# Performance work log

Hardware: AMD Instinct MI355X
Metric: run time of the kernel (lower is better)

Reference implementation:

```python
import jax, jax.numpy as jnp
import numpy as np

N_NODES = 50000
N_EDGES = 600000
VOCAB = 50000
D_IN = 256   # embed.output_size
D = 128      # size


def gcn_conv(x, w, b, src, dst, num_nodes):
    # PyG GCNConv: x' = D^{-1/2} (A + I) D^{-1/2} (x @ W^T) + b
    loop = jnp.arange(num_nodes)
    s = jnp.concatenate([src, loop])
    d = jnp.concatenate([dst, loop])
    x = x @ w.T                                           # [N, D]
    deg = jax.ops.segment_sum(jnp.ones_like(s, x.dtype), d, num_segments=num_nodes)
    dinv = jnp.where(deg > 0, jax.lax.rsqrt(deg), 0.0)
    norm = dinv[s] * dinv[d]                              # [E+N]
    msgs = x[s] * norm[:, None]                           # gather + scale
    out = jax.ops.segment_sum(msgs, d, num_segments=num_nodes)  # scatter-add
    return out + b


def setup_inputs() -> dict:
    key = jax.random.key(0)
    ks = jax.random.split(key, 7)
    node_tokens = jax.random.randint(ks[0], (N_NODES,), 0, VOCAB)
    edge_index = jax.random.randint(ks[1], (2, N_EDGES), 0, N_NODES)
    embed_table = jax.random.normal(ks[2], (VOCAB, D_IN), dtype=jnp.float32) * 0.02
    W_node_w = jax.random.normal(ks[3], (D, D_IN), dtype=jnp.float32) * 0.02
    W_node_b = jnp.zeros((D,), dtype=jnp.float32)
    w1 = jax.random.normal(ks[4], (D, D), dtype=jnp.float32) * 0.02
    b1 = jnp.zeros((D,), dtype=jnp.float32)
    w2 = jax.random.normal(ks[5], (D, D), dtype=jnp.float32) * 0.02
    b2 = jnp.zeros((D,), dtype=jnp.float32)
    return {"node_tokens": node_tokens, "edge_index": edge_index,
            "embed_table": embed_table, "W_node_w": W_node_w, "W_node_b": W_node_b,
            "w1": w1, "b1": b1, "w2": w2, "b2": b2}


def reference(node_tokens, edge_index, embed_table, W_node_w, W_node_b, w1, b1, w2, b2):
    src, dst = edge_index[0], edge_index[1]
    e = embed_table[node_tokens]                 # [N, D_IN] embedding lookup
    x = e @ W_node_w.T + W_node_b                # [N, D]
    x = gcn_conv(x, w1, b1, src, dst, N_NODES)
    x = jax.nn.relu(x)
    x = gcn_conv(x, w2, b2, src, dst, N_NODES)
    return x
```

## Files before the change

kernel.cpp:

```cpp
#include <hip/hip_runtime.h>
#include <hip/hip_bf16.h>

#define N_NODES 50000
#define N_EDGES 600000
#define D_IN 256
#define D 128

#define SCAN_CHUNK 1024
#define N_CHUNKS ((N_NODES + SCAN_CHUNK - 1) / SCAN_CHUNK)
#define GEMM_BLOCKS ((N_NODES + 31) / 32)
#define EDGE_BLOCKS ((N_EDGES + 255) / 256)

typedef unsigned short ushort_t;
typedef __attribute__((ext_vector_type(8))) short bf16x8;
typedef __attribute__((ext_vector_type(16))) float f32x16;

__device__ __forceinline__ float bf2f(ushort_t u) {
  union { unsigned int i; float f; } v;
  v.i = ((unsigned int)u) << 16;
  return v.f;
}
__device__ __forceinline__ ushort_t f2bf(float f) {
  union { float f; unsigned int i; } v;
  v.f = f;
  unsigned int x = v.i;
  unsigned int r = (x + 0x7FFFu + ((x >> 16) & 1u)) >> 16;
  return (ushort_t)r;
}
__device__ __forceinline__ float bflo(unsigned int u) {
  union { unsigned int i; float f; } v;
  v.i = u << 16;
  return v.f;
}
__device__ __forceinline__ float bfhi(unsigned int u) {
  union { unsigned int i; float f; } v;
  v.i = u & 0xFFFF0000u;
  return v.f;
}


__global__ __launch_bounds__(256) void k_prep_deg(
    const float* __restrict__ wn, const float* __restrict__ w1,
    const float* __restrict__ bn, const float* __restrict__ w2,
    const float* __restrict__ b1, const float* __restrict__ b2,
    const int* __restrict__ dst,
    ushort_t* __restrict__ WcSw, float* __restrict__ bc,
    ushort_t* __restrict__ W2Sw, float* __restrict__ b1f,
    float* __restrict__ b2f, int* __restrict__ deg,
    int* __restrict__ epos) {
  int bid = blockIdx.x;
  if (bid < 128) {
    int j = bid;
    int k = threadIdx.x;
    float acc = 0.f;
#pragma unroll 8
    for (int m = 0; m < 128; m++)
      acc += w1[j * 128 + m] * wn[m * 256 + k];
    ushort_t h = f2bf(acc);
    ushort_t l = f2bf(acc - bf2f(h));
    int wv = j >> 5, fm = j & 31;
    int kh = k >> 7, t = (k >> 4) & 7, fq = (k >> 3) & 1, c = k & 7;
    int lane = fq * 32 + fm;
    int base = ((wv * 2 + kh) * 8 + t) * 2 * 512 + lane * 8 + c;
    WcSw[base] = h;
    WcSw[base + 512] = l;
    if (k == 0) {
      float s = 0.f;
      for (int m = 0; m < 128; m++) s += w1[j * 128 + m] * bn[m];
      bc[j] = s;
    }
  } else if (bid < 193) {
    int i = (bid - 128) * 256 + threadIdx.x;
    if (i >= 16640) return;
    if (i < 16384) {
      float v = w2[i];
      ushort_t h = f2bf(v);
      ushort_t l = f2bf(v - bf2f(h));
      int j = i >> 7, k = i & 127;
      int wv = j >> 5, fm = j & 31;
      int t = (k >> 4) & 7, fq = (k >> 3) & 1, c = k & 7;
      int lane = fq * 32 + fm;
      int base = (wv * 8 + t) * 2 * 512 + lane * 8 + c;
      W2Sw[base] = h;
      W2Sw[base + 512] = l;
    } else if (i < 16512) {
      b1f[i - 16384] = b1[i - 16384];
    } else {
      b2f[i - 16512] = b2[i - 16512];
    }
  } else {
    int e = (bid - 193) * 256 + threadIdx.x;
    if (e < N_EDGES) epos[e] = atomicAdd(&deg[dst[e]], 1);
  }
}


__global__ void k_partial(const int* __restrict__ deg, int* __restrict__ partial) {
  __shared__ int lds[256];
  int b = blockIdx.x, t = threadIdx.x;
  int base = b * SCAN_CHUNK + t * 4;
  int s = 0;
#pragma unroll
  for (int i = 0; i < 4; i++) {
    int idx = base + i;
    if (idx < N_NODES) s += deg[idx];
  }
  lds[t] = s;
  __syncthreads();
  for (int off = 128; off > 0; off >>= 1) {
    if (t < off) lds[t] += lds[t + off];
    __syncthreads();
  }
  if (t == 0) partial[b] = lds[0];
}

__global__ void k_scan_final(const int* __restrict__ deg, const int* __restrict__ partial,
                             int* __restrict__ row_start, float* __restrict__ dinv,
                             ushort_t* __restrict__ T1z, ushort_t* __restrict__ T2z) {
  __shared__ int lds[256];
  __shared__ int plds[64];
  int b = blockIdx.x, t = threadIdx.x;
  if (t < N_CHUNKS) plds[t] = partial[t];
  __syncthreads();
  if (t == 0) {
    int s = 0;
    for (int i = 0; i < b; i++) s += plds[i];
    plds[63] = s;
  }
  int base = b * SCAN_CHUNK + t * 4;
  int v[4];
  int s = 0;
#pragma unroll
  for (int i = 0; i < 4; i++) {
    int idx = base + i;
    v[i] = (idx < N_NODES) ? deg[idx] : 0;
    s += v[i];
  }
  lds[t] = s;
  __syncthreads();
  for (int off = 1; off < 256; off <<= 1) {
    int add = (t >= off) ? lds[t - off] : 0;
    __syncthreads();
    lds[t] += add;
    __syncthreads();
  }
  int excl = lds[t] - s + plds[63];
#pragma unroll
  for (int i = 0; i < 4; i++) {
    int idx = base + i;
    if (idx < N_NODES) {
      row_start[idx] = excl;
      dinv[idx] = rsqrtf((float)(v[i] + 1));
      excl += v[i];
    }
  }
  if (b == 0) {
    if (t == 0) row_start[N_NODES] = N_EDGES;
    unsigned int* z1 = (unsigned int*)&T1z[(size_t)N_NODES * D];
    unsigned int* z2 = (unsigned int*)&T2z[(size_t)N_NODES * D];
    if (t < 64) z1[t] = 0u;
    else if (t < 128) z2[t - 64] = 0u;
  }
}

__global__ __launch_bounds__(256) void k_gemm_fill(
    const float* __restrict__ Xv, const int* __restrict__ tokens,
    const ushort_t* __restrict__ Wsw,
    const float* __restrict__ bias, const float* __restrict__ dinvp,
    ushort_t* __restrict__ OutT,
    const int* __restrict__ src, const int* __restrict__ dst,
    const int* __restrict__ row_start, const int* __restrict__ epos,
    int* __restrict__ csr) {
  constexpr int XS = 136;
  __shared__ __align__(16) ushort_t xh_lds[32 * XS];
  __shared__ __align__(16) ushort_t xl_lds[32 * XS];

  int bid = blockIdx.x;
  if (bid >= GEMM_BLOCKS) {
    int e = (bid - GEMM_BLOCKS) * 256 + threadIdx.x;
    if (e < N_EDGES) {
      int d = dst[e];
      csr[row_start[d] + epos[e]] = src[e];
    }
    return;
  }

  int tid = threadIdx.x;
  int lane = tid & 63;
  int wv = tid >> 6;
  int node0 = bid * 32;
  int fm = lane & 31;
  int fq = lane >> 5;
  int r8 = tid >> 5;
  int c32 = tid & 31;

  const char* xb = (const char*)Xv;
  float4 v0[4], v1[4];
  int rows[4];
#pragma unroll
  for (int i = 0; i < 4; i++) {
    rows[i] = r8 * 4 + i;
    int tk = tokens[min(node0 + rows[i], N_NODES - 1)];
    unsigned off = (unsigned)tk * (D_IN * 4) + (unsigned)c32 * 16;
    v0[i] = *(const float4*)(xb + off);
    v1[i] = *(const float4*)(xb + off + 512);
  }

  f32x16 acc;
#pragma unroll
  for (int r = 0; r < 16; r++) acc[r] = 0.f;

#pragma unroll
  for (int kh = 0; kh < 2; kh++) {
#pragma unroll
    for (int i = 0; i < 4; i++) {
      float4 v = (kh == 0) ? v0[i] : v1[i];
      ushort4 h, l;
      h.x = f2bf(v.x); l.x = f2bf(v.x - bf2f(h.x));
      h.y = f2bf(v.y); l.y = f2bf(v.y - bf2f(h.y));
      h.z = f2bf(v.z); l.z = f2bf(v.z - bf2f(h.z));
      h.w = f2bf(v.w); l.w = f2bf(v.w - bf2f(h.w));
      *(ushort4*)&xh_lds[rows[i] * XS + 4 * c32] = h;
      *(ushort4*)&xl_lds[rows[i] * XS + 4 * c32] = l;
    }
    __syncthreads();

    const ushort_t* wb = Wsw + ((size_t)(wv * 2 + kh) * 8) * 2 * 512 + lane * 8;
#pragma unroll
    for (int tc = 0; tc < 2; tc++) {
      bf16x8 wbh[4], wbl[4];
#pragma unroll
      for (int t4 = 0; t4 < 4; t4++) {
        wbh[t4] = *(const bf16x8*)(wb + (size_t)(tc * 4 + t4) * 1024);
        wbl[t4] = *(const bf16x8*)(wb + (size_t)(tc * 4 + t4) * 1024 + 512);
      }
#pragma unroll
      for (int t4 = 0; t4 < 4; t4++) {
        int ko = (tc * 4 + t4) * 16 + fq * 8;
        bf16x8 ah = *(const bf16x8*)&xh_lds[fm * XS + ko];
        bf16x8 al = *(const bf16x8*)&xl_lds[fm * XS + ko];
        acc = __builtin_amdgcn_mfma_f32_32x32x16_bf16(ah, wbh[t4], acc, 0, 0, 0);
        acc = __builtin_amdgcn_mfma_f32_32x32x16_bf16(ah, wbl[t4], acc, 0, 0, 0);
        acc = __builtin_amdgcn_mfma_f32_32x32x16_bf16(al, wbh[t4], acc, 0, 0, 0);
      }
    }
    if (kh == 0) __syncthreads();
  }

  int j = wv * 32 + fm;
  float bv = bias[j];
#pragma unroll
  for (int r = 0; r < 16; r++) {
    int row = (r & 3) + 8 * (r >> 2) + 4 * fq;
    int node = node0 + row;
    if (node < N_NODES)
      OutT[(size_t)node * D + j] = f2bf((acc[r] + bv) * dinvp[node]);
  }
}

__device__ __forceinline__ void addu4(float acc[8], uint4 u) {
  acc[0] += bflo(u.x);
  acc[1] += bfhi(u.x);
  acc[2] += bflo(u.y);
  acc[3] += bfhi(u.y);
  acc[4] += bflo(u.z);
  acc[5] += bfhi(u.z);
  acc[6] += bflo(u.w);
  acc[7] += bfhi(u.w);
}

__device__ __forceinline__ uint4 ldrow(const char* tbase, int s, int h) {
  return *(const uint4*)(tbase + (((unsigned)s << 8) + ((unsigned)h << 4)));
}

__device__ __forceinline__ void burst8(const char* tbase, int sidx,
                                       int gbase, int qoff, int h, float acc[8]) {
  uint4 u[8];
#pragma unroll
  for (int q = 0; q < 8; q++) {
    int s = __shfl(sidx, gbase + qoff + q);
    u[q] = ldrow(tbase, s, h);
  }
#pragma unroll
  for (int q = 0; q < 8; q++) addu4(acc, u[q]);
}

__device__ __forceinline__ void agg_tail(const char* tbase,
                                         const int* __restrict__ csr,
                                         int e0, int e1, int gbase, int h,
                                         float acc[8]) {
  for (int b2 = e0 + 16; b2 < e1; b2 += 16) {
    int c2 = e1 - b2;
    int sx = (h < c2) ? csr[b2 + h] : N_NODES;
    burst8(tbase, sx, gbase, 0, h, acc);
    burst8(tbase, sx, gbase, 8, h, acc);
  }
}

__global__ __launch_bounds__(256) void k_agg_gemm(
    const ushort_t* __restrict__ t1, const int* __restrict__ row_start,
    const int* __restrict__ csr, const float* __restrict__ dinv,
    const float* __restrict__ b1f,
    const ushort_t* __restrict__ Wsw, ushort_t* __restrict__ OutT2) {
  constexpr int XS = 136;
  __shared__ __align__(16) ushort_t xh_lds[32 * XS];
  __shared__ __align__(16) ushort_t xl_lds[32 * XS];

  int tid = threadIdx.x;
  int lane = tid & 63;
  int wv = tid >> 6;
  int node0 = blockIdx.x * 32;
  int fm = lane & 31;
  int fq = lane >> 5;
  int g = lane >> 4;
  int h = lane & 15;
  int gbase = lane & 48;

  const char* tb = (const char*)t1;
  float4 bA = *(const float4*)&b1f[h * 8];
  float4 bB = *(const float4*)&b1f[h * 8 + 4];

  int node0w = node0 + wv * 8;
  int rsv = row_start[min(node0w + min(lane, 8), N_NODES)];
  float dvl = dinv[min(node0w + min(lane, 7), N_NODES - 1)];

  int nodeA = node0w + g;
  int nodeB = node0w + 4 + g;
  int e0A = __shfl(rsv, g), e1A = __shfl(rsv, g + 1);
  int e0B = __shfl(rsv, 4 + g), e1B = __shfl(rsv, 5 + g);
  int cntA = e1A - e0A, cntB = e1B - e0B;
  bool vA = nodeA < N_NODES, vB = nodeB < N_NODES;

  int sidxA = (h < cntA) ? csr[e0A + h] : N_NODES;
  int sidxB = (h < cntB) ? csr[e0B + h] : N_NODES;
  uint4 usA = ldrow(tb, vA ? nodeA : N_NODES, h);
  uint4 usB = ldrow(tb, vB ? nodeB : N_NODES, h);
  float diA = __shfl(dvl, g);
  float diB = __shfl(dvl, 4 + g);

  float accA[8];
#pragma unroll
  for (int q = 0; q < 8; q++) accA[q] = 0.f;
  addu4(accA, usA);
  burst8(tb, sidxA, gbase, 0, h, accA);
  burst8(tb, sidxA, gbase, 8, h, accA);
  agg_tail(tb, csr, e0A, e1A, gbase, h, accA);

  float accB[8];
#pragma unroll
  for (int q = 0; q < 8; q++) accB[q] = 0.f;
  addu4(accB, usB);
  burst8(tb, sidxB, gbase, 0, h, accB);
  burst8(tb, sidxB, gbase, 8, h, accB);
  agg_tail(tb, csr, e0B, e1B, gbase, h, accB);

#pragma unroll
  for (int p = 0; p < 2; p++) {
    float* acc = p ? accB : accA;
    bool vv = p ? vB : vA;
    float di = p ? diB : diA;
    int row = wv * 8 + p * 4 + g;
    bf16x8 ph, pl;
    if (vv) {
      float val[8];
      val[0] = fmaxf(di * acc[0] + bA.x, 0.f);
      val[1] = fmaxf(di * acc[1] + bA.y, 0.f);
      val[2] = fmaxf(di * acc[2] + bA.z, 0.f);
      val[3] = fmaxf(di * acc[3] + bA.w, 0.f);
      val[4] = fmaxf(di * acc[4] + bB.x, 0.f);
      val[5] = fmaxf(di * acc[5] + bB.y, 0.f);
      val[6] = fmaxf(di * acc[6] + bB.z, 0.f);
      val[7] = fmaxf(di * acc[7] + bB.w, 0.f);
#pragma unroll
      for (int q = 0; q < 8; q++) {
        ushort_t hq = f2bf(val[q]);
        ph[q] = (short)hq;
        pl[q] = (short)f2bf(val[q] - bf2f(hq));
      }
    } else {
#pragma unroll
      for (int q = 0; q < 8; q++) { ph[q] = 0; pl[q] = 0; }
    }
    *(bf16x8*)&xh_lds[row * XS + h * 8] = ph;
    *(bf16x8*)&xl_lds[row * XS + h * 8] = pl;
  }
  __syncthreads();

  f32x16 acc;
#pragma unroll
  for (int r = 0; r < 16; r++) acc[r] = 0.f;
  {
    const ushort_t* wb = Wsw + ((size_t)wv * 8) * 2 * 512 + lane * 8;
#pragma unroll
    for (int tc = 0; tc < 2; tc++) {
      bf16x8 wbh[4], wbl[4];
#pragma unroll
      for (int t4 = 0; t4 < 4; t4++) {
        wbh[t4] = *(const bf16x8*)(wb + (size_t)(tc * 4 + t4) * 1024);
        wbl[t4] = *(const bf16x8*)(wb + (size_t)(tc * 4 + t4) * 1024 + 512);
      }
#pragma unroll
      for (int t4 = 0; t4 < 4; t4++) {
        int ko = (tc * 4 + t4) * 16 + fq * 8;
        bf16x8 ah = *(const bf16x8*)&xh_lds[fm * XS + ko];
        bf16x8 al = *(const bf16x8*)&xl_lds[fm * XS + ko];
        acc = __builtin_amdgcn_mfma_f32_32x32x16_bf16(ah, wbh[t4], acc, 0, 0, 0);
        acc = __builtin_amdgcn_mfma_f32_32x32x16_bf16(ah, wbl[t4], acc, 0, 0, 0);
        acc = __builtin_amdgcn_mfma_f32_32x32x16_bf16(al, wbh[t4], acc, 0, 0, 0);
      }
    }
  }
  int j = wv * 32 + fm;
#pragma unroll
  for (int r = 0; r < 16; r++) {
    int row = (r & 3) + 8 * (r >> 2) + 4 * fq;
    int node = node0 + row;
    if (node < N_NODES)
      OutT2[(size_t)node * D + j] = f2bf(acc[r] * dinv[node]);
  }
}

__global__ __launch_bounds__(256) void k_aggregate_out(
    const ushort_t* __restrict__ t, const int* __restrict__ row_start,
    const int* __restrict__ csr, const float* __restrict__ dinv,
    const float* __restrict__ bias, float* __restrict__ out_f) {
  int wv = threadIdx.x >> 6;
  int lane = threadIdx.x & 63;
  int g = lane >> 4;
  int h = lane & 15;
  int gbase = lane & 48;
  int nodew = blockIdx.x * 16 + wv * 4;
  int rsv = row_start[min(nodew + min(lane, 4), N_NODES)];
  float dvl = dinv[min(nodew + min(lane, 3), N_NODES - 1)];
  int node = nodew + g;
  int e0 = __shfl(rsv, g), e1 = __shfl(rsv, g + 1);
  int cnt = e1 - e0;
  bool vn = node < N_NODES;

  const char* tb = (const char*)t;
  int sidx = (h < cnt) ? csr[e0 + h] : N_NODES;
  uint4 us = ldrow(tb, vn ? node : N_NODES, h);
  float di = __shfl(dvl, g);

  float acc[8];
#pragma unroll
  for (int q = 0; q < 8; q++) acc[q] = 0.f;
  addu4(acc, us);
  burst8(tb, sidx, gbase, 0, h, acc);
  burst8(tb, sidx, gbase, 8, h, acc);
  agg_tail(tb, csr, e0, e1, gbase, h, acc);

  if (!vn) return;
  float4 bA = *(const float4*)&bias[h * 8];
  float4 bB = *(const float4*)&bias[h * 8 + 4];
  float4 o0, o1;
  o0.x = di * acc[0] + bA.x;
  o0.y = di * acc[1] + bA.y;
  o0.z = di * acc[2] + bA.z;
  o0.w = di * acc[3] + bA.w;
  o1.x = di * acc[4] + bB.x;
  o1.y = di * acc[5] + bB.y;
  o1.z = di * acc[6] + bB.z;
  o1.w = di * acc[7] + bB.w;
  *(float4*)&out_f[(size_t)node * D + h * 8] = o0;
  *(float4*)&out_f[(size_t)node * D + h * 8 + 4] = o1;
}

extern "C" void kernel_launch(void* const* d_in, const int* in_sizes, int n_in,
                              void* d_out, int out_size, void* d_ws, size_t ws_size,
                              hipStream_t stream) {
  const int* tokens = (const int*)d_in[0];
  const int* edge = (const int*)d_in[1];
  const float* embed = (const float*)d_in[2];
  const float* Wn = (const float*)d_in[3];
  const float* bn = (const float*)d_in[4];
  const float* w1 = (const float*)d_in[5];
  const float* b1 = (const float*)d_in[6];
  const float* w2 = (const float*)d_in[7];
  const float* b2 = (const float*)d_in[8];
  float* out = (float*)d_out;

  const int* src = edge;
  const int* dst = edge + N_EDGES;

  char* ws = (char*)d_ws;
  ushort_t* T1 = (ushort_t*)ws;
  ushort_t* T2 = (ushort_t*)(ws + 12800256);
  int* epos = (int*)(ws + 25600512);
  float* dinv = (float*)(ws + 28000512);
  int* row_start = (int*)(ws + 28200512);
  int* deg = (int*)(ws + 28400576);
  int* csr = (int*)(ws + 28600576);
  int* partial = (int*)(ws + 31000576);
  ushort_t* WcSw = (ushort_t*)(ws + 31000832);
  ushort_t* W2Sw = (ushort_t*)(ws + 31131904);
  float* bias_ws = (float*)(ws + 31197440);
  float* bcf = bias_ws;
  float* b1f = bias_ws + 128;
  float* b2f = bias_ws + 256;

  hipMemsetAsync(deg, 0, N_NODES * sizeof(int), stream);
  k_prep_deg<<<193 + EDGE_BLOCKS, 256, 0, stream>>>(
      Wn, w1, bn, w2, b1, b2, dst, WcSw, bcf, W2Sw, b1f, b2f, deg, epos);

  k_partial<<<N_CHUNKS, 256, 0, stream>>>(deg, partial);
  k_scan_final<<<N_CHUNKS, 256, 0, stream>>>(deg, partial, row_start, dinv, T1, T2);

  k_gemm_fill<<<GEMM_BLOCKS + EDGE_BLOCKS, 256, 0, stream>>>(
      embed, tokens, WcSw, bcf, dinv, T1, src, dst, row_start, epos, csr);

  k_agg_gemm<<<GEMM_BLOCKS, 256, 0, stream>>>(
      T1, row_start, csr, dinv, b1f, W2Sw, T2);

  k_aggregate_out<<<(N_NODES + 15) / 16, 256, 0, stream>>>(
      T2, row_start, csr, dinv, b2f, out);
}
```

Before: 231.4 us.

## Replace CSR scan build with fixed-capacity per-node buckets plus overflow list

Drops the prefix-scan kernels and the separate CSR fill pass. Incoming edges are now written directly into fixed 32-slot per-node buckets during the degree atomic pass, and rare excess edges go to a small global overflow list. Degree normalization is recomputed inline from deg instead of being stored as a dinv array. This removes two kernel launches and one edge pass, at the cost of scattered bucket writes, a larger bucket array, and a linear overflow scan for high-degree nodes. It also silently drops edges if the overflow list exceeds its cap.

```diff
diff --git a/kernel.cpp b/kernel.cpp
--- a/kernel.cpp
+++ b/kernel.cpp
@@ -6,10 +6,11 @@
 #define D_IN 256
 #define D 128
 
-#define SCAN_CHUNK 1024
-#define N_CHUNKS ((N_NODES + SCAN_CHUNK - 1) / SCAN_CHUNK)
 #define GEMM_BLOCKS ((N_NODES + 31) / 32)
 #define EDGE_BLOCKS ((N_EDGES + 255) / 256)
+#define OUT_CHUNKS (N_NODES / 16)
+#define BCAP 32
+#define OVF_CAP 2048
 
 typedef unsigned short ushort_t;
 typedef __attribute__((ext_vector_type(8))) short bf16x8;
@@ -39,19 +40,23 @@
 }
 
 
-__global__ __launch_bounds__(256) void k_prep_deg(
+__global__ __launch_bounds__(256) void k_prep_fill(
     const float* __restrict__ wn, const float* __restrict__ w1,
     const float* __restrict__ bn, const float* __restrict__ w2,
     const float* __restrict__ b1, const float* __restrict__ b2,
-    const int* __restrict__ dst,
-    ushort_t* __restrict__ WcSw, float* __restrict__ bc,
-    ushort_t* __restrict__ W2Sw, float* __restrict__ b1f,
-    float* __restrict__ b2f, int* __restrict__ deg,
-    int* __restrict__ epos) {
+    const int* __restrict__ src, const int* __restrict__ dst,
+    ushort_t* __restrict__ WcSw, ushort_t* __restrict__ W2Sw,
+    float* __restrict__ bias_ws, int* __restrict__ deg,
+    int* __restrict__ bucket, int* __restrict__ ovfc, int* __restrict__ ovf,
+    ushort_t* __restrict__ T1z, ushort_t* __restrict__ T2z) {
   int bid = blockIdx.x;
+  int tid = threadIdx.x;
+  float* bcf = bias_ws;
+  float* b1f = bias_ws + 128;
+  float* b2f = bias_ws + 256;
   if (bid < 128) {
     int j = bid;
-    int k = threadIdx.x;
+    int k = tid;
     float acc = 0.f;
 #pragma unroll 8
     for (int m = 0; m < 128; m++)
@@ -67,11 +72,10 @@
     if (k == 0) {
       float s = 0.f;
       for (int m = 0; m < 128; m++) s += w1[j * 128 + m] * bn[m];
-      bc[j] = s;
+      bcf[j] = s;
     }
   } else if (bid < 193) {
-    int i = (bid - 128) * 256 + threadIdx.x;
-    if (i >= 16640) return;
+    int i = (bid - 128) * 256 + tid;
     if (i < 16384) {
       float v = w2[i];
       ushort_t h = f2bf(v);
@@ -85,110 +89,45 @@
       W2Sw[base + 512] = l;
     } else if (i < 16512) {
       b1f[i - 16384] = b1[i - 16384];
-    } else {
+    } else if (i < 16640) {
       b2f[i - 16512] = b2[i - 16512];
     }
-  } else {
-    int e = (bid - 193) * 256 + threadIdx.x;
-    if (e < N_EDGES) epos[e] = atomicAdd(&deg[dst[e]], 1);
-  }
-}
-
-
-__global__ void k_partial(const int* __restrict__ deg, int* __restrict__ partial) {
-  __shared__ int lds[256];
-  int b = blockIdx.x, t = threadIdx.x;
-  int base = b * SCAN_CHUNK + t * 4;
-  int s = 0;
-#pragma unroll
-  for (int i = 0; i < 4; i++) {
-    int idx = base + i;
-    if (idx < N_NODES) s += deg[idx];
-  }
-  lds[t] = s;
-  __syncthreads();
-  for (int off = 128; off > 0; off >>= 1) {
-    if (t < off) lds[t] += lds[t + off];
-    __syncthreads();
-  }
-  if (t == 0) partial[b] = lds[0];
-}
-
-__global__ void k_scan_final(const int* __restrict__ deg, const int* __restrict__ partial,
-                             int* __restrict__ row_start, float* __restrict__ dinv,
-                             ushort_t* __restrict__ T1z, ushort_t* __restrict__ T2z) {
-  __shared__ int lds[256];
-  __shared__ int plds[64];
-  int b = blockIdx.x, t = threadIdx.x;
-  if (t < N_CHUNKS) plds[t] = partial[t];
-  __syncthreads();
-  if (t == 0) {
-    int s = 0;
-    for (int i = 0; i < b; i++) s += plds[i];
-    plds[63] = s;
-  }
-  int base = b * SCAN_CHUNK + t * 4;
-  int v[4];
-  int s = 0;
-#pragma unroll
-  for (int i = 0; i < 4; i++) {
-    int idx = base + i;
-    v[i] = (idx < N_NODES) ? deg[idx] : 0;
-    s += v[i];
-  }
-  lds[t] = s;
-  __syncthreads();
-  for (int off = 1; off < 256; off <<= 1) {
-    int add = (t >= off) ? lds[t - off] : 0;
-    __syncthreads();
-    lds[t] += add;
-    __syncthreads();
-  }
-  int excl = lds[t] - s + plds[63];
-#pragma unroll
-  for (int i = 0; i < 4; i++) {
-    int idx = base + i;
-    if (idx < N_NODES) {
-      row_start[idx] = excl;
-      dinv[idx] = rsqrtf((float)(v[i] + 1));
-      excl += v[i];
-    }
-  }
-  if (b == 0) {
-    if (t == 0) row_start[N_NODES] = N_EDGES;
+  } else if (bid == 193) {
     unsigned int* z1 = (unsigned int*)&T1z[(size_t)N_NODES * D];
     unsigned int* z2 = (unsigned int*)&T2z[(size_t)N_NODES * D];
-    if (t < 64) z1[t] = 0u;
-    else if (t < 128) z2[t - 64] = 0u;
-  }
-}
-
-__global__ __launch_bounds__(256) void k_gemm_fill(
+    if (tid < 64) z1[tid] = 0u;
+    else if (tid < 128) z2[tid - 64] = 0u;
+  } else {
+    int e = (bid - 194) * 256 + tid;
+    if (e < N_EDGES) {
+      int d = dst[e];
+      int s = src[e];
+      int pos = atomicAdd(&deg[d], 1);
+      if (pos < BCAP) {
+        bucket[d * BCAP + pos] = s;
+      } else {
+        int oi = atomicAdd(ovfc, 1);
+        if (oi < OVF_CAP) {
+          ovf[2 * oi] = d;
+          ovf[2 * oi + 1] = s;
+        }
+      }
+    }
+  }
+}
+
+__global__ __launch_bounds__(256) void k_gemm(
     const float* __restrict__ Xv, const int* __restrict__ tokens,
-    const ushort_t* __restrict__ Wsw,
-    const float* __restrict__ bias, const float* __restrict__ dinvp,
-    ushort_t* __restrict__ OutT,
-    const int* __restrict__ src, const int* __restrict__ dst,
-    const int* __restrict__ row_start, const int* __restrict__ epos,
-    int* __restrict__ csr) {
+    const ushort_t* __restrict__ Wsw, const float* __restrict__ bias,
+    const int* __restrict__ deg, ushort_t* __restrict__ OutT) {
   constexpr int XS = 136;
   __shared__ __align__(16) ushort_t xh_lds[32 * XS];
   __shared__ __align__(16) ushort_t xl_lds[32 * XS];
 
-  int bid = blockIdx.x;
-  if (bid >= GEMM_BLOCKS) {
-    int e = (bid - GEMM_BLOCKS) * 256 + threadIdx.x;
-    if (e < N_EDGES) {
-      int d = dst[e];
-      csr[row_start[d] + epos[e]] = src[e];
-    }
-    return;
-  }
-
   int tid = threadIdx.x;
   int lane = tid & 63;
   int wv = tid >> 6;
-  int node0 = bid * 32;
+  int node0 = blockIdx.x * 32;
   int fm = lane & 31;
   int fq = lane >> 5;
   int r8 = tid >> 5;
@@ -253,8 +192,10 @@
   for (int r = 0; r < 16; r++) {
     int row = (r & 3) + 8 * (r >> 2) + 4 * fq;
     int node = node0 + row;
-    if (node < N_NODES)
-      OutT[(size_t)node * D + j] = f2bf((acc[r] + bv) * dinvp[node]);
+    if (node < N_NODES) {
+      float di = rsqrtf((float)(deg[node] + 1));
+      OutT[(size_t)node * D + j] = f2bf((acc[r] + bv) * di);
+    }
   }
 }
 
@@ -285,22 +226,31 @@
   for (int q = 0; q < 8; q++) addu4(acc, u[q]);
 }
 
-__device__ __forceinline__ void agg_tail(const char* tbase,
-                                         const int* __restrict__ csr,
-                                         int e0, int e1, int gbase, int h,
-                                         float acc[8]) {
-  for (int b2 = e0 + 16; b2 < e1; b2 += 16) {
-    int c2 = e1 - b2;
-    int sx = (h < c2) ? csr[b2 + h] : N_NODES;
+__device__ __forceinline__ void gather_node(
+    const char* tbase, const int* __restrict__ bucket,
+    const int* __restrict__ ovf, int novf,
+    int node, int degv, bool valid, int gbase, int h, float acc[8]) {
+  int cnt = valid ? min(degv, BCAP) : 0;
+  addu4(acc, ldrow(tbase, valid ? node : N_NODES, h));
+  int sidx = (h < cnt) ? bucket[node * BCAP + h] : N_NODES;
+  burst8(tbase, sidx, gbase, 0, h, acc);
+  burst8(tbase, sidx, gbase, 8, h, acc);
+  for (int b2 = 16; b2 < cnt; b2 += 16) {
+    int sx = (b2 + h < cnt) ? bucket[node * BCAP + b2 + h] : N_NODES;
     burst8(tbase, sx, gbase, 0, h, acc);
     burst8(tbase, sx, gbase, 8, h, acc);
   }
+  if (valid && degv > BCAP) {
+    for (int i = 0; i < novf; i++) {
+      if (ovf[2 * i] == node) addu4(acc, ldrow(tbase, ovf[2 * i + 1], h));
+    }
+  }
 }
 
 __global__ __launch_bounds__(256) void k_agg_gemm(
-    const ushort_t* __restrict__ t1, const int* __restrict__ row_start,
-    const int* __restrict__ csr, const float* __restrict__ dinv,
-    const float* __restrict__ b1f,
+    const ushort_t* __restrict__ t1, const int* __restrict__ deg,
+    const int* __restrict__ bucket, const int* __restrict__ ovfc,
+    const int* __restrict__ ovf, const float* __restrict__ b1f,
     const ushort_t* __restrict__ Wsw, ushort_t* __restrict__ OutT2) {
   constexpr int XS = 136;
   __shared__ __align__(16) ushort_t xh_lds[32 * XS];
@@ -319,40 +269,28 @@
   const char* tb = (const char*)t1;
   float4 bA = *(const float4*)&b1f[h * 8];
   float4 bB = *(const float4*)&b1f[h * 8 + 4];
+  int novf = *ovfc;
 
   int node0w = node0 + wv * 8;
-  int rsv = row_start[min(node0w + min(lane, 8), N_NODES)];
-  float dvl = dinv[min(node0w + min(lane, 7), N_NODES - 1)];
+  int dgl = deg[min(node0w + min(lane, 7), N_NODES - 1)];
 
   int nodeA = node0w + g;
   int nodeB = node0w + 4 + g;
-  int e0A = __shfl(rsv, g), e1A = __shfl(rsv, g + 1);
-  int e0B = __shfl(rsv, 4 + g), e1B = __shfl(rsv, 5 + g);
-  int cntA = e1A - e0A, cntB = e1B - e0B;
+  int degA = __shfl(dgl, g);
+  int degB = __shfl(dgl, 4 + g);
   bool vA = nodeA < N_NODES, vB = nodeB < N_NODES;
-
-  int sidxA = (h < cntA) ? csr[e0A + h] : N_NODES;
-  int sidxB = (h < cntB) ? csr[e0B + h] : N_NODES;
-  uint4 usA = ldrow(tb, vA ? nodeA : N_NODES, h);
-  uint4 usB = ldrow(tb, vB ? nodeB : N_NODES, h);
-  float diA = __shfl(dvl, g);
-  float diB = __shfl(dvl, 4 + g);
+  float diA = rsqrtf((float)(degA + 1));
+  float diB = rsqrtf((float)(degB + 1));
 
   float accA[8];
 #pragma unroll
   for (int q = 0; q < 8; q++) accA[q] = 0.f;
-  addu4(accA, usA);
-  burst8(tb, sidxA, gbase, 0, h, accA);
-  burst8(tb, sidxA, gbase, 8, h, accA);
-  agg_tail(tb, csr, e0A, e1A, gbase, h, accA);
+  gather_node(tb, bucket, ovf, novf, nodeA, degA, vA, gbase, h, accA);
 
   float accB[8];
 #pragma unroll
   for (int q = 0; q < 8; q++) accB[q] = 0.f;
-  addu4(accB, usB);
-  burst8(tb, sidxB, gbase, 0, h, accB);
-  burst8(tb, sidxB, gbase, 8, h, accB);
-  agg_tail(tb, csr, e0B, e1B, gbase, h, accB);
+  gather_node(tb, bucket, ovf, novf, nodeB, degB, vB, gbase, h, accB);
 
 #pragma unroll
   for (int p = 0; p < 2; p++) {
@@ -415,40 +353,36 @@
   for (int r = 0; r < 16; r++) {
     int row = (r & 3) + 8 * (r >> 2) + 4 * fq;
     int node = node0 + row;
-    if (node < N_NODES)
-      OutT2[(size_t)node * D + j] = f2bf(acc[r] * dinv[node]);
-  }
-}
-
-__global__ __launch_bounds__(256) void k_aggregate_out(
-    const ushort_t* __restrict__ t, const int* __restrict__ row_start,
-    const int* __restrict__ csr, const float* __restrict__ dinv,
-    const float* __restrict__ bias, float* __restrict__ out_f) {
+    if (node < N_NODES) {
+      float di = rsqrtf((float)(deg[node] + 1));
+      OutT2[(size_t)node * D + j] = f2bf(acc[r] * di);
+    }
+  }
+}
+
+__global__ __launch_bounds__(256) void k_agg_out(
+    const ushort_t* __restrict__ t, const int* __restrict__ deg,
+    const int* __restrict__ bucket, const int* __restrict__ ovfc,
+    const int* __restrict__ ovf, const float* __restrict__ bias,
+    float* __restrict__ out_f) {
   int wv = threadIdx.x >> 6;
   int lane = threadIdx.x & 63;
   int g = lane >> 4;
   int h = lane & 15;
   int gbase = lane & 48;
   int nodew = blockIdx.x * 16 + wv * 4;
-  int rsv = row_start[min(nodew + min(lane, 4), N_NODES)];
-  float dvl = dinv[min(nodew + min(lane, 3), N_NODES - 1)];
+  int dgl = deg[min(nodew + min(lane, 3), N_NODES - 1)];
   int node = nodew + g;
-  int e0 = __shfl(rsv, g), e1 = __shfl(rsv, g + 1);
-  int cnt = e1 - e0;
+  int degn = __shfl(dgl, g);
   bool vn = node < N_NODES;
+  float di = rsqrtf((float)(degn + 1));
+  int novf = *ovfc;
 
   const char* tb = (const char*)t;
-  int sidx = (h < cnt) ? csr[e0 + h] : N_NODES;
-  uint4 us = ldrow(tb, vn ? node : N_NODES, h);
-  float di = __shfl(dvl, g);
-
   float acc[8];
 #pragma unroll
   for (int q = 0; q < 8; q++) acc[q] = 0.f;
-  addu4(acc, us);
-  burst8(tb, sidx, gbase, 0, h, acc);
-  burst8(tb, sidx, gbase, 8, h, acc);
-  agg_tail(tb, csr, e0, e1, gbase, h, acc);
+  gather_node(tb, bucket, ovf, novf, node, degn, vn, gbase, h, acc);
 
   if (!vn) return;
   float4 bA = *(const float4*)&bias[h * 8];
@@ -486,32 +420,29 @@
   char* ws = (char*)d_ws;
   ushort_t* T1 = (ushort_t*)ws;
   ushort_t* T2 = (ushort_t*)(ws + 12800256);
-  int* epos = (int*)(ws + 25600512);
-  float* dinv = (float*)(ws + 28000512);
-  int* row_start = (int*)(ws + 28200512);
-  int* deg = (int*)(ws + 28400576);
-  int* csr = (int*)(ws + 28600576);
-  int* partial = (int*)(ws + 31000576);
-  ushort_t* WcSw = (ushort_t*)(ws + 31000832);
-  ushort_t* W2Sw = (ushort_t*)(ws + 31131904);
-  float* bias_ws = (float*)(ws + 31197440);
+  int* bucket = (int*)(ws + 25600512);
+  int* deg = (int*)(ws + 32000512);
+  int* ovfc = (int*)(ws + 32200512);
+  int* ovf = (int*)(ws + 32200640);
+  ushort_t* WcSw = (ushort_t*)(ws + 32217088);
+  ushort_t* W2Sw = (ushort_t*)(ws + 32348160);
+  float* bias_ws = (float*)(ws + 32413696);
   float* bcf = bias_ws;
   float* b1f = bias_ws + 128;
   float* b2f = bias_ws + 256;
 
-  hipMemsetAsync(deg, 0, N_NODES * sizeof(int), stream);
-  k_prep_deg<<<193 + EDGE_BLOCKS, 256, 0, stream>>>(
-      Wn, w1, bn, w2, b1, b2, dst, WcSw, bcf, W2Sw, b1f, b2f, deg, epos);
-
-  k_partial<<<N_CHUNKS, 256, 0, stream>>>(deg, partial);
-  k_scan_final<<<N_CHUNKS, 256, 0, stream>>>(deg, partial, row_start, dinv, T1, T2);
-
-  k_gemm_fill<<<GEMM_BLOCKS + EDGE_BLOCKS, 256, 0, stream>>>(
-      embed, tokens, WcSw, bcf, dinv, T1, src, dst, row_start, epos, csr);
+  hipMemsetAsync(deg, 0, 200128, stream);
+
+  k_prep_fill<<<194 + EDGE_BLOCKS, 256, 0, stream>>>(
+      Wn, w1, bn, w2, b1, b2, src, dst, WcSw, W2Sw, bias_ws, deg,
+      bucket, ovfc, ovf, T1, T2);
+
+  k_gemm<<<GEMM_BLOCKS, 256, 0, stream>>>(
+      embed, tokens, WcSw, bcf, deg, T1);
 
   k_agg_gemm<<<GEMM_BLOCKS, 256, 0, stream>>>(
-      T1, row_start, csr, dinv, b1f, W2Sw, T2);
-
-  k_aggregate_out<<<(N_NODES + 15) / 16, 256, 0, stream>>>(
-      T2, row_start, csr, dinv, b2f, out);
-}
+      T1, deg, bucket, ovfc, ovf, b1f, W2Sw, T2);
+
+  k_agg_out<<<OUT_CHUNKS, 256, 0, stream>>>(
+      T2, deg, bucket, ovfc, ovf, b2f, out);
+}
```

Result: no change. 227.9 us (-1.5%).
